# Kernel optimization log

Hardware: AMD Instinct MI355X
Metric: run time of the kernel (lower is better)

## Reference

```python
import jax, jax.numpy as jnp
import numpy as np

D_MODEL = 1024
H = 16
D_K = D_MODEL // H
VOCAB = 2048            # ctor arg `max_relative_position` actually sets embedding vocab size
MAX_REL_POS = 1000      # hardcoded in the original module
B = 4
S = 1024


def setup_inputs() -> dict:
    key = jax.random.key(0)
    ks = jax.random.split(key, 13)
    sc = 1.0 / np.sqrt(D_MODEL)
    inp = {
        "query": jax.random.normal(ks[0], (B, S, D_MODEL), jnp.float32),
        "key": jax.random.normal(ks[1], (B, S, D_MODEL), jnp.float32),
        "value": jax.random.normal(ks[2], (B, S, D_MODEL), jnp.float32),
        "Wq": jax.random.normal(ks[3], (D_MODEL, D_MODEL), jnp.float32) * sc,
        "bq": jnp.zeros((D_MODEL,), jnp.float32),
        "Wk": jax.random.normal(ks[4], (D_MODEL, D_MODEL), jnp.float32) * sc,
        "bk": jnp.zeros((D_MODEL,), jnp.float32),
        "Wv": jax.random.normal(ks[5], (D_MODEL, D_MODEL), jnp.float32) * sc,
        "bv": jnp.zeros((D_MODEL,), jnp.float32),
        "Wo": jax.random.normal(ks[6], (D_MODEL, D_MODEL), jnp.float32) * sc,
        "bo": jnp.zeros((D_MODEL,), jnp.float32),
        "embK": jax.random.normal(ks[7], (VOCAB, D_K), jnp.float32),
        "embV": jax.random.normal(ks[8], (VOCAB, D_K), jnp.float32),
    }
    return inp


def _rel_pos_idx(seq_len):
    r = jnp.arange(seq_len)
    dist = r[None, :] - r[:, None]                       # [S, S]
    return jnp.clip(dist, -MAX_REL_POS, MAX_REL_POS) + MAX_REL_POS


def reference(query, key, value, Wq, bq, Wk, bk, Wv, bv, Wo, bo, embK, embV):
    b, s, _ = query.shape
    proj = lambda x, W, bias: (x @ W.T + bias).reshape(b, s, H, D_K).transpose(0, 2, 1, 3)
    q = proj(query, Wq, bq)   # [B, H, S, Dk]
    k = proj(key, Wk, bk)
    v = proj(value, Wv, bv)

    idx = _rel_pos_idx(s)                                # [S, S] int
    rk = embK[idx]                                       # [S, S, Dk]
    rv = embV[idx]                                       # [S, S, Dk]

    # logits = Q K^T + Q R_K^T (Shaw-style, no 1/sqrt(dk) scaling in original)
    logits = jnp.einsum("bhqd,bhkd->bhqk", q, k) + jnp.einsum("bhqd,qkd->bhqk", q, rk)
    weights = jax.nn.softmax(logits, axis=-1)            # dropout is identity in eval

    # x = W V + W R_V
    x = jnp.einsum("bhqk,bhkd->bhqd", weights, v) + jnp.einsum("bhqk,qkd->bhqd", weights, rv)
    x = x.transpose(0, 2, 1, 3).reshape(b, s, H * D_K)
    out = x @ Wo.T + bo
    return out, weights
```

## Files before the change

kernel.cpp:

```cpp
#include <hip/hip_runtime.h>
#include <math.h>

#define Bn   4
#define Sn   1024
#define Dn   1024
#define Hn   16
#define DKn  64
#define MRPn 1000
#define RKU  2049

typedef __attribute__((ext_vector_type(8))) short short8;
typedef __attribute__((ext_vector_type(4))) float f32x4;

static __device__ __forceinline__ unsigned short f2bf(float f) {
    unsigned u = __float_as_uint(f);
    u += 0x7FFF + ((u >> 16) & 1);
    return (unsigned short)(u >> 16);
}
static __device__ __forceinline__ float bf2f(unsigned short h) {
    return __uint_as_float((unsigned)h << 16);
}

__global__ __launch_bounds__(256) void cast_f32_bf16(
    const float* __restrict__ s, unsigned short* __restrict__ d, int n)
{
    int i = (blockIdx.x * 256 + threadIdx.x) * 4;
    if (i >= n) return;
    float4 v = *(const float4*)(s + i);
    ushort4 o;
    o.x = f2bf(v.x); o.y = f2bf(v.y); o.z = f2bf(v.z); o.w = f2bf(v.w);
    *(ushort4*)(d + i) = o;
}

#define LP 40
__global__ __launch_bounds__(256) void gemm_bf16_mfma(
    const unsigned short* __restrict__ A, const unsigned short* __restrict__ W,
    const float* __restrict__ bias, float* __restrict__ C,
    unsigned short* __restrict__ Chi, unsigned short* __restrict__ Clo,
    int M, int N, int K, int mode)
{
    __shared__ unsigned short As[128 * LP];
    __shared__ unsigned short Bs[128 * LP];
    const int tid  = threadIdx.x;
    const int lane = tid & 63;
    const int wave = tid >> 6;
    const int m0 = blockIdx.y * 128, n0 = blockIdx.x * 128;
    const int wm = (wave & 1) * 64, wn = (wave >> 1) * 64;
    const int fr   = lane & 15;
    const int quad = lane >> 4;

    f32x4 acc[4][4];
#pragma unroll
    for (int i = 0; i < 4; ++i)
#pragma unroll
        for (int j = 0; j < 4; ++j) acc[i][j] = (f32x4){0.f, 0.f, 0.f, 0.f};

    const int srow   = tid >> 2;
    const int schunk = (tid & 3) * 8;

    for (int kb = 0; kb < K; kb += 32) {
        const unsigned short* ga = A + (size_t)(m0 + srow) * K + kb + schunk;
        const unsigned short* gb = W + (size_t)(n0 + srow) * K + kb + schunk;
        short8 a0 = *(const short8*)ga;
        short8 a1 = *(const short8*)(ga + (size_t)64 * K);
        short8 b0 = *(const short8*)gb;
        short8 b1 = *(const short8*)(gb + (size_t)64 * K);
        __syncthreads();
        *(short8*)&As[srow * LP + schunk]        = a0;
        *(short8*)&As[(srow + 64) * LP + schunk] = a1;
        *(short8*)&Bs[srow * LP + schunk]        = b0;
        *(short8*)&Bs[(srow + 64) * LP + schunk] = b1;
        __syncthreads();

        short8 af[4], bf[4];
#pragma unroll
        for (int mi = 0; mi < 4; ++mi)
            af[mi] = *(const short8*)&As[(wm + 16 * mi + fr) * LP + quad * 8];
#pragma unroll
        for (int ni = 0; ni < 4; ++ni)
            bf[ni] = *(const short8*)&Bs[(wn + 16 * ni + fr) * LP + quad * 8];
#pragma unroll
        for (int mi = 0; mi < 4; ++mi)
#pragma unroll
            for (int ni = 0; ni < 4; ++ni)
                acc[mi][ni] = __builtin_amdgcn_mfma_f32_16x16x32_bf16(
                    af[mi], bf[ni], acc[mi][ni], 0, 0, 0);
    }

    if (mode == 0) {
#pragma unroll
        for (int ni = 0; ni < 4; ++ni) {
            int cc = n0 + wn + 16 * ni + fr;
            float bv = bias[cc];
#pragma unroll
            for (int mi = 0; mi < 4; ++mi) {
                int rbase = m0 + wm + 16 * mi + quad * 4;
#pragma unroll
                for (int r = 0; r < 4; ++r)
                    C[(size_t)(rbase + r) * N + cc] = acc[mi][ni][r] + bv;
            }
        }
    } else if (mode == 1) {
#pragma unroll
        for (int ni = 0; ni < 4; ++ni) {
            int cc = n0 + wn + 16 * ni + fr;
            int h = cc >> 6, d = cc & 63;
            float bv = bias[cc];
#pragma unroll
            for (int mi = 0; mi < 4; ++mi) {
                int rbase = m0 + wm + 16 * mi + quad * 4;
                int b = rbase >> 10, q0 = rbase & 1023;
#pragma unroll
                for (int r = 0; r < 4; ++r) {
                    float val = acc[mi][ni][r] + bv;
                    unsigned short hi = f2bf(val);
                    unsigned short lo = f2bf(val - bf2f(hi));
                    size_t o = (((size_t)b * Hn + h) * Sn + q0 + r) * DKn + d;
                    Chi[o] = hi; Clo[o] = lo;
                }
            }
        }
    } else {
#pragma unroll
        for (int ni = 0; ni < 4; ++ni) {
            int cc = n0 + wn + 16 * ni + fr;
            int h = cc >> 6, d = cc & 63;
            float bv = bias[cc];
#pragma unroll
            for (int mi = 0; mi < 4; ++mi) {
                int rbase = m0 + wm + 16 * mi + quad * 4;
                int b = rbase >> 10, tok0 = rbase & 1023;
                ushort4 o4;
#pragma unroll
                for (int r = 0; r < 4; ++r) o4[r] = f2bf(acc[mi][ni][r] + bv);
                *(ushort4*)&Chi[(((size_t)b * Hn + h) * DKn + d) * Sn + tok0] = o4;
            }
        }
    }
}

__global__ __launch_bounds__(256) void build_rk(
    const float* __restrict__ embK, unsigned short* __restrict__ Rh,
    unsigned short* __restrict__ Rl)
{
    int i = (blockIdx.x * 256 + threadIdx.x) * 4;
    if (i >= RKU * DKn) return;
    int u = i >> 6, d0 = i & 63;
    int t = min(max(u - 1024, -MRPn), MRPn);
    float4 v = *(const float4*)&embK[(size_t)(t + MRPn) * DKn + d0];
    ushort4 hi, lo;
    hi.x = f2bf(v.x); lo.x = f2bf(v.x - bf2f(hi.x));
    hi.y = f2bf(v.y); lo.y = f2bf(v.y - bf2f(hi.y));
    hi.z = f2bf(v.z); lo.z = f2bf(v.z - bf2f(hi.z));
    hi.w = f2bf(v.w); lo.w = f2bf(v.w - bf2f(hi.w));
    *(ushort4*)&Rh[i] = hi;
    *(ushort4*)&Rl[i] = lo;
}

__global__ __launch_bounds__(256) void build_e2v(
    const float* __restrict__ embV, unsigned short* __restrict__ E2V)
{
    int i = (blockIdx.x * 256 + threadIdx.x) * 8;
    int d = i >> 11, u0 = i & 2047;
    short8 o;
#pragma unroll
    for (int e = 0; e < 8; ++e) {
        int t = u0 + e - 1024;
        t = min(max(t, -MRPn), MRPn);
        o[e] = (short)f2bf(embV[(size_t)(t + MRPn) * DKn + d]);
    }
    *(short8*)&E2V[i] = o;
}

__global__ __launch_bounds__(256) void logits_mfma(
    const unsigned short* __restrict__ Qh, const unsigned short* __restrict__ Ql,
    const unsigned short* __restrict__ Kh, const unsigned short* __restrict__ Kl,
    const unsigned short* __restrict__ Rh, const unsigned short* __restrict__ Rl,
    float* __restrict__ L)
{
    __shared__ float RelU[64][132];
    const int tid = threadIdx.x;
    const int lane = tid & 63, wave = tid >> 6;
    const int wy = wave >> 1, wx = wave & 1;
    const int fr = lane & 15, quad = lane >> 4;
    const int n = blockIdx.x;
    const int virt = (n & 7) * 128 + (n >> 3);
    const int bh = virt >> 4, q0 = (virt & 15) * 64;

    const unsigned short* qbh = Qh + ((size_t)bh * Sn + q0) * DKn;
    const unsigned short* qbl = Ql + ((size_t)bh * Sn + q0) * DKn;

    short8 aH[2][2], aL[2][2];
#pragma unroll
    for (int kbi = 0; kbi < 2; ++kbi)
#pragma unroll
        for (int mi = 0; mi < 2; ++mi) {
            int off = (wy * 32 + 16 * mi + fr) * DKn + kbi * 32 + quad * 8;
            aH[kbi][mi] = *(const short8*)(qbh + off);
            aL[kbi][mi] = *(const short8*)(qbl + off);
        }

    for (int kt = 0; kt < 16; ++kt) {
        const int k0 = kt * 64;
        const unsigned short* kbh = Kh + ((size_t)bh * Sn + k0) * DKn;
        const unsigned short* kbl = Kl + ((size_t)bh * Sn + k0) * DKn;
        const int u0 = k0 - q0 + 961 + wx * 64;
        const unsigned short* rbh = Rh + (size_t)u0 * DKn;
        const unsigned short* rbl = Rl + (size_t)u0 * DKn;

        f32x4 acc[2][2], rel[2][4];
#pragma unroll
        for (int i = 0; i < 2; ++i)
#pragma unroll
            for (int j = 0; j < 2; ++j) acc[i][j] = (f32x4){0.f, 0.f, 0.f, 0.f};
#pragma unroll
        for (int i = 0; i < 2; ++i)
#pragma unroll
            for (int j = 0; j < 4; ++j) rel[i][j] = (f32x4){0.f, 0.f, 0.f, 0.f};

#pragma unroll
        for (int kbi = 0; kbi < 2; ++kbi) {
            short8 bKH[2], bKL[2], bRH[4], bRL[4];
#pragma unroll
            for (int ni = 0; ni < 2; ++ni) {
                int off = (wx * 32 + 16 * ni + fr) * DKn + kbi * 32 + quad * 8;
                bKH[ni] = *(const short8*)(kbh + off);
                bKL[ni] = *(const short8*)(kbl + off);
            }
#pragma unroll
            for (int ni = 0; ni < 4; ++ni) {
                int off = (16 * ni + fr) * DKn + kbi * 32 + quad * 8;
                bRH[ni] = *(const short8*)(rbh + off);
                bRL[ni] = *(const short8*)(rbl + off);
            }
#pragma unroll
            for (int mi = 0; mi < 2; ++mi)
#pragma unroll
                for (int ni = 0; ni < 2; ++ni) {
                    acc[mi][ni] = __builtin_amdgcn_mfma_f32_16x16x32_bf16(
                        aH[kbi][mi], bKH[ni], acc[mi][ni], 0, 0, 0);
                    acc[mi][ni] = __builtin_amdgcn_mfma_f32_16x16x32_bf16(
                        aL[kbi][mi], bKH[ni], acc[mi][ni], 0, 0, 0);
                    acc[mi][ni] = __builtin_amdgcn_mfma_f32_16x16x32_bf16(
                        aH[kbi][mi], bKL[ni], acc[mi][ni], 0, 0, 0);
                }
#pragma unroll
            for (int mi = 0; mi < 2; ++mi)
#pragma unroll
                for (int ni = 0; ni < 4; ++ni) {
                    rel[mi][ni] = __builtin_amdgcn_mfma_f32_16x16x32_bf16(
                        aH[kbi][mi], bRH[ni], rel[mi][ni], 0, 0, 0);
                    rel[mi][ni] = __builtin_amdgcn_mfma_f32_16x16x32_bf16(
                        aL[kbi][mi], bRH[ni], rel[mi][ni], 0, 0, 0);
                    rel[mi][ni] = __builtin_amdgcn_mfma_f32_16x16x32_bf16(
                        aH[kbi][mi], bRL[ni], rel[mi][ni], 0, 0, 0);
                }
        }

#pragma unroll
        for (int mi = 0; mi < 2; ++mi)
#pragma unroll
            for (int ni = 0; ni < 4; ++ni)
#pragma unroll
                for (int r = 0; r < 4; ++r)
                    RelU[wy * 32 + 16 * mi + quad * 4 + r]
                        [wx * 64 + 16 * ni + fr] = rel[mi][ni][r];
        __syncthreads();
#pragma unroll
        for (int mi = 0; mi < 2; ++mi)
#pragma unroll
            for (int ni = 0; ni < 2; ++ni) {
                int c = wx * 32 + 16 * ni + fr;
#pragma unroll
                for (int r = 0; r < 4; ++r) {
                    int row = wy * 32 + 16 * mi + quad * 4 + r;
                    L[((size_t)bh * Sn + q0 + row) * Sn + k0 + c] =
                        acc[mi][ni][r] + RelU[row][c - row + 63];
                }
            }
        __syncthreads();
    }
}

__global__ __launch_bounds__(256) void softmax_kernel(float* __restrict__ Wt)
{
    __shared__ float red[4];
    const int tid = threadIdx.x;
    float* p = Wt + (size_t)blockIdx.x * Sn;
    float4 v = ((const float4*)p)[tid];

    float m = fmaxf(fmaxf(v.x, v.y), fmaxf(v.z, v.w));
#pragma unroll
    for (int o = 32; o > 0; o >>= 1) m = fmaxf(m, __shfl_down(m, o, 64));
    if ((tid & 63) == 0) red[tid >> 6] = m;
    __syncthreads();
    m = fmaxf(fmaxf(red[0], red[1]), fmaxf(red[2], red[3]));
    __syncthreads();

    float4 e;
    e.x = expf(v.x - m); e.y = expf(v.y - m);
    e.z = expf(v.z - m); e.w = expf(v.w - m);
    float s = e.x + e.y + e.z + e.w;
#pragma unroll
    for (int o = 32; o > 0; o >>= 1) s += __shfl_down(s, o, 64);
    if ((tid & 63) == 0) red[tid >> 6] = s;
    __syncthreads();
    s = red[0] + red[1] + red[2] + red[3];

    float inv = 1.0f / s;
    e.x *= inv; e.y *= inv; e.z *= inv; e.w *= inv;
    ((float4*)p)[tid] = e;
}

__global__ __launch_bounds__(256) void av_mfma(
    const float* __restrict__ Wt, const unsigned short* __restrict__ Vt,
    const unsigned short* __restrict__ E2V, unsigned short* __restrict__ Xbf)
{
    __shared__ unsigned short As[64 * LP];
    __shared__ unsigned short Bs[64 * LP];
    const int tid  = threadIdx.x;
    const int lane = tid & 63;
    const int wave = tid >> 6;
    const int q0 = blockIdx.x * 64;
    const int bh = blockIdx.y;
    const int b = bh >> 4, h = bh & 15;
    const int wm = (wave & 1) * 32;
    const int wn = (wave >> 1) * 32;
    const int fr = lane & 15, quad = lane >> 4;

    const float* Wrow = Wt + (size_t)bh * Sn * Sn;

    f32x4 acc[2][2];
#pragma unroll
    for (int i = 0; i < 2; ++i)
#pragma unroll
        for (int j = 0; j < 2; ++j) acc[i][j] = (f32x4){0.f, 0.f, 0.f, 0.f};

    const int ar = tid >> 3;
    const int ac = (tid & 7) * 4;
    const int br = tid >> 2;
    const int bc = (tid & 3) * 8;

    const unsigned short* vrow = Vt + ((size_t)bh * DKn + br) * Sn;

    for (int kb = 0; kb < Sn; kb += 32) {
        short8 bv = *(const short8*)(vrow + kb + bc);
        float4 a0 = *(const float4*)&Wrow[(size_t)(q0 + ar) * Sn + kb + ac];
        float4 a1 = *(const float4*)&Wrow[(size_t)(q0 + ar + 32) * Sn + kb + ac];
        __syncthreads();
        ushort4 s0, s1;
        s0.x = f2bf(a0.x); s0.y = f2bf(a0.y); s0.z = f2bf(a0.z); s0.w = f2bf(a0.w);
        s1.x = f2bf(a1.x); s1.y = f2bf(a1.y); s1.z = f2bf(a1.z); s1.w = f2bf(a1.w);
        *(ushort4*)&As[ar * LP + ac]        = s0;
        *(ushort4*)&As[(ar + 32) * LP + ac] = s1;
        *(short8*)&Bs[br * LP + bc]         = bv;
        __syncthreads();

        short8 af[2], bfv[2];
#pragma unroll
        for (int mi = 0; mi < 2; ++mi)
            af[mi] = *(const short8*)&As[(wm + 16 * mi + fr) * LP + quad * 8];
#pragma unroll
        for (int ni = 0; ni < 2; ++ni)
            bfv[ni] = *(const short8*)&Bs[(wn + 16 * ni + fr) * LP + quad * 8];
#pragma unroll
        for (int mi = 0; mi < 2; ++mi)
#pragma unroll
            for (int ni = 0; ni < 2; ++ni)
                acc[mi][ni] = __builtin_amdgcn_mfma_f32_16x16x32_bf16(
                    af[mi], bfv[ni], acc[mi][ni], 0, 0, 0);
    }

    int lo = 1024 - q0 - 63; if (lo < 0) lo = 0; lo &= ~31;
    const int hi = 2047 - q0;
    for (int ub = lo; ub <= hi; ub += 32) {
        short8 bv = *(const short8*)&E2V[(size_t)br * 2048 + ub + bc];
        float fa[2][4];
#pragma unroll
        for (int p = 0; p < 2; ++p) {
            int q = q0 + ar + 32 * p;
            int k = q + ub + ac - 1024;
#pragma unroll
            for (int e = 0; e < 4; ++e) {
                int ke = k + e;
                fa[p][e] = ((unsigned)ke < 1024u) ? Wrow[(size_t)q * Sn + ke] : 0.f;
            }
        }
        __syncthreads();
        ushort4 s0, s1;
        s0.x = f2bf(fa[0][0]); s0.y = f2bf(fa[0][1]);
        s0.z = f2bf(fa[0][2]); s0.w = f2bf(fa[0][3]);
        s1.x = f2bf(fa[1][0]); s1.y = f2bf(fa[1][1]);
        s1.z = f2bf(fa[1][2]); s1.w = f2bf(fa[1][3]);
        *(ushort4*)&As[ar * LP + ac]        = s0;
        *(ushort4*)&As[(ar + 32) * LP + ac] = s1;
        *(short8*)&Bs[br * LP + bc]         = bv;
        __syncthreads();

        short8 af[2], bfv[2];
#pragma unroll
        for (int mi = 0; mi < 2; ++mi)
            af[mi] = *(const short8*)&As[(wm + 16 * mi + fr) * LP + quad * 8];
#pragma unroll
        for (int ni = 0; ni < 2; ++ni)
            bfv[ni] = *(const short8*)&Bs[(wn + 16 * ni + fr) * LP + quad * 8];
#pragma unroll
        for (int mi = 0; mi < 2; ++mi)
#pragma unroll
            for (int ni = 0; ni < 2; ++ni)
                acc[mi][ni] = __builtin_amdgcn_mfma_f32_16x16x32_bf16(
                    af[mi], bfv[ni], acc[mi][ni], 0, 0, 0);
    }

#pragma unroll
    for (int ni = 0; ni < 2; ++ni) {
        int d = wn + 16 * ni + fr;
#pragma unroll
        for (int mi = 0; mi < 2; ++mi) {
            int qb = q0 + wm + 16 * mi + quad * 4;
#pragma unroll
            for (int r = 0; r < 4; ++r)
                Xbf[(size_t)(b * Sn + qb + r) * Dn + h * DKn + d] =
                    f2bf(acc[mi][ni][r]);
        }
    }
}

extern "C" void kernel_launch(void* const* d_in, const int* in_sizes, int n_in,
                              void* d_out, int out_size, void* d_ws, size_t ws_size,
                              hipStream_t stream)
{
    const float* query = (const float*)d_in[0];
    const float* key   = (const float*)d_in[1];
    const float* value = (const float*)d_in[2];
    const float* Wq    = (const float*)d_in[3];
    const float* bq    = (const float*)d_in[4];
    const float* Wk    = (const float*)d_in[5];
    const float* bk    = (const float*)d_in[6];
    const float* Wv    = (const float*)d_in[7];
    const float* bv    = (const float*)d_in[8];
    const float* Wo    = (const float*)d_in[9];
    const float* bo    = (const float*)d_in[10];
    const float* embK  = (const float*)d_in[11];
    const float* embV  = (const float*)d_in[12];

    const size_t NTOK = (size_t)Bn * Sn;
    const size_t PROJ = NTOK * Dn;
    const size_t WSZ  = (size_t)Dn * Dn;

    unsigned short* u16 = (unsigned short*)d_ws;
    unsigned short* Abf = u16;
    unsigned short* Wqb = Abf + PROJ;
    unsigned short* Wkb = Wqb + WSZ;
    unsigned short* Wvb = Wkb + WSZ;
    unsigned short* Wob = Wvb + WSZ;
    unsigned short* Qhi = Wob + WSZ;
    unsigned short* Qlo = Qhi + PROJ;
    unsigned short* Khi = Qlo + PROJ;
    unsigned short* Klo = Khi + PROJ;
    unsigned short* Vtb = Klo + PROJ;
    unsigned short* E2V = Vtb + PROJ;
    unsigned short* RkH = E2V + (size_t)DKn * 2048;
    unsigned short* RkL = RkH + (size_t)RKU * DKn;

    float* outp = (float*)d_out;
    float* Wt   = outp + PROJ;

    const int CAST_W_GRID = (int)(WSZ / 4 / 256);
    const int CAST_A_GRID = (int)(PROJ / 4 / 256);
    dim3 gemmGrid(Dn / 128, (int)(NTOK / 128));

    build_e2v<<<64, 256, 0, stream>>>(embV, E2V);
    build_rk<<<(RKU * DKn / 4 + 255) / 256, 256, 0, stream>>>(embK, RkH, RkL);

    cast_f32_bf16<<<CAST_W_GRID, 256, 0, stream>>>(Wq, Wqb, (int)WSZ);
    cast_f32_bf16<<<CAST_W_GRID, 256, 0, stream>>>(Wk, Wkb, (int)WSZ);
    cast_f32_bf16<<<CAST_W_GRID, 256, 0, stream>>>(Wv, Wvb, (int)WSZ);
    cast_f32_bf16<<<CAST_W_GRID, 256, 0, stream>>>(Wo, Wob, (int)WSZ);

    cast_f32_bf16<<<CAST_A_GRID, 256, 0, stream>>>(query, Abf, (int)PROJ);
    gemm_bf16_mfma<<<gemmGrid, 256, 0, stream>>>(Abf, Wqb, bq, nullptr, Qhi, Qlo,
                                                 (int)NTOK, Dn, Dn, 1);
    cast_f32_bf16<<<CAST_A_GRID, 256, 0, stream>>>(key, Abf, (int)PROJ);
    gemm_bf16_mfma<<<gemmGrid, 256, 0, stream>>>(Abf, Wkb, bk, nullptr, Khi, Klo,
                                                 (int)NTOK, Dn, Dn, 1);
    cast_f32_bf16<<<CAST_A_GRID, 256, 0, stream>>>(value, Abf, (int)PROJ);
    gemm_bf16_mfma<<<gemmGrid, 256, 0, stream>>>(Abf, Wvb, bv, nullptr, Vtb, nullptr,
                                                 (int)NTOK, Dn, Dn, 2);

    logits_mfma<<<Bn * Hn * (Sn / 64), 256, 0, stream>>>(
        Qhi, Qlo, Khi, Klo, RkH, RkL, Wt);

    softmax_kernel<<<Bn * Hn * Sn, 256, 0, stream>>>(Wt);

    av_mfma<<<dim3(Sn / 64, Bn * Hn), 256, 0, stream>>>(Wt, Vtb, E2V, Abf);

    gemm_bf16_mfma<<<gemmGrid, 256, 0, stream>>>(Abf, Wob, bo, outp, nullptr, nullptr,
                                                 (int)NTOK, Dn, Dn, 0);
}
```

Baseline: 890.0 us.

## Fuse logits, softmax and attention-value product into one attention kernel

```diff
diff --git a/kernel.cpp b/kernel.cpp
--- a/kernel.cpp
+++ b/kernel.cpp
@@ -8,6 +8,7 @@
 #define DKn  64
 #define MRPn 1000
 #define RKU  2049
+#define EP   2112
 
 typedef __attribute__((ext_vector_type(8))) short short8;
 typedef __attribute__((ext_vector_type(4))) float f32x4;
@@ -161,7 +162,8 @@
     const float* __restrict__ embV, unsigned short* __restrict__ E2V)
 {
     int i = (blockIdx.x * 256 + threadIdx.x) * 8;
-    int d = i >> 11, u0 = i & 2047;
+    if (i >= DKn * EP) return;
+    int d = i / EP, u0 = i % EP;
     short8 o;
 #pragma unroll
     for (int e = 0; e < 8; ++e) {
@@ -172,256 +174,230 @@
     *(short8*)&E2V[i] = o;
 }
 
-__global__ __launch_bounds__(256) void logits_mfma(
+__global__ __launch_bounds__(256) void attn_fused(
     const unsigned short* __restrict__ Qh, const unsigned short* __restrict__ Ql,
     const unsigned short* __restrict__ Kh, const unsigned short* __restrict__ Kl,
     const unsigned short* __restrict__ Rh, const unsigned short* __restrict__ Rl,
-    float* __restrict__ L)
-{
-    __shared__ float RelU[64][132];
+    const unsigned short* __restrict__ Vt, const unsigned short* __restrict__ E2V,
+    float* __restrict__ Lw, unsigned short* __restrict__ Xbf)
+{
+    __shared__ unsigned short Pbuf[32][1032];
+    __shared__ __align__(16) char scratch[12800];
+    __shared__ float rowred[32][2];
+    __shared__ float mrun[32], srun[32];
+    __shared__ float mts[16][32];
+
+    float (*RelU)[100] = (float(*)[100])scratch;
+    float (*ftab)[32]  = (float(*)[32])scratch;
+    unsigned short (*Ssk)[72] = (unsigned short(*)[72])(scratch + 2048);
+
     const int tid = threadIdx.x;
     const int lane = tid & 63, wave = tid >> 6;
     const int wy = wave >> 1, wx = wave & 1;
     const int fr = lane & 15, quad = lane >> 4;
     const int n = blockIdx.x;
-    const int virt = (n & 7) * 128 + (n >> 3);
-    const int bh = virt >> 4, q0 = (virt & 15) * 64;
-
-    const unsigned short* qbh = Qh + ((size_t)bh * Sn + q0) * DKn;
-    const unsigned short* qbl = Ql + ((size_t)bh * Sn + q0) * DKn;
-
-    short8 aH[2][2], aL[2][2];
-#pragma unroll
-    for (int kbi = 0; kbi < 2; ++kbi)
-#pragma unroll
-        for (int mi = 0; mi < 2; ++mi) {
-            int off = (wy * 32 + 16 * mi + fr) * DKn + kbi * 32 + quad * 8;
-            aH[kbi][mi] = *(const short8*)(qbh + off);
-            aL[kbi][mi] = *(const short8*)(qbl + off);
-        }
+    const int virt = (n & 7) * 256 + (n >> 3);
+    const int bh = virt >> 5, q0 = (virt & 31) * 32;
+
+    if (tid < 32) { mrun[tid] = -INFINITY; srun[tid] = 0.f; }
+
+    const unsigned short* qbh = Qh + ((size_t)bh * Sn + q0 + wy * 16 + fr) * DKn;
+    const unsigned short* qbl = Ql + ((size_t)bh * Sn + q0 + wy * 16 + fr) * DKn;
+    short8 aH[2], aL[2];
+#pragma unroll
+    for (int kbi = 0; kbi < 2; ++kbi) {
+        aH[kbi] = *(const short8*)(qbh + kbi * 32 + quad * 8);
+        aL[kbi] = *(const short8*)(qbl + kbi * 32 + quad * 8);
+    }
 
     for (int kt = 0; kt < 16; ++kt) {
         const int k0 = kt * 64;
-        const unsigned short* kbh = Kh + ((size_t)bh * Sn + k0) * DKn;
-        const unsigned short* kbl = Kl + ((size_t)bh * Sn + k0) * DKn;
-        const int u0 = k0 - q0 + 961 + wx * 64;
-        const unsigned short* rbh = Rh + (size_t)u0 * DKn;
-        const unsigned short* rbl = Rl + (size_t)u0 * DKn;
-
-        f32x4 acc[2][2], rel[2][4];
-#pragma unroll
-        for (int i = 0; i < 2; ++i)
-#pragma unroll
-            for (int j = 0; j < 2; ++j) acc[i][j] = (f32x4){0.f, 0.f, 0.f, 0.f};
-#pragma unroll
-        for (int i = 0; i < 2; ++i)
-#pragma unroll
-            for (int j = 0; j < 4; ++j) rel[i][j] = (f32x4){0.f, 0.f, 0.f, 0.f};
+        const unsigned short* kbh = Kh + ((size_t)bh * Sn + k0 + wx * 32 + fr) * DKn;
+        const unsigned short* kbl = Kl + ((size_t)bh * Sn + k0 + wx * 32 + fr) * DKn;
+        const int ubase = k0 - q0 + 993;
+        const unsigned short* rbh = Rh + ((size_t)(ubase + wx * 48) + fr) * DKn;
+        const unsigned short* rbl = Rl + ((size_t)(ubase + wx * 48) + fr) * DKn;
+
+        f32x4 acc2[2], rel3[3];
+#pragma unroll
+        for (int i = 0; i < 2; ++i) acc2[i] = (f32x4){0.f, 0.f, 0.f, 0.f};
+#pragma unroll
+        for (int i = 0; i < 3; ++i) rel3[i] = (f32x4){0.f, 0.f, 0.f, 0.f};
 
 #pragma unroll
         for (int kbi = 0; kbi < 2; ++kbi) {
-            short8 bKH[2], bKL[2], bRH[4], bRL[4];
+            short8 bKH[2], bKL[2], bRH[3], bRL[3];
 #pragma unroll
             for (int ni = 0; ni < 2; ++ni) {
-                int off = (wx * 32 + 16 * ni + fr) * DKn + kbi * 32 + quad * 8;
+                size_t off = (size_t)16 * ni * DKn + kbi * 32 + quad * 8;
                 bKH[ni] = *(const short8*)(kbh + off);
                 bKL[ni] = *(const short8*)(kbl + off);
             }
 #pragma unroll
-            for (int ni = 0; ni < 4; ++ni) {
-                int off = (16 * ni + fr) * DKn + kbi * 32 + quad * 8;
+            for (int ni = 0; ni < 3; ++ni) {
+                size_t off = (size_t)16 * ni * DKn + kbi * 32 + quad * 8;
                 bRH[ni] = *(const short8*)(rbh + off);
                 bRL[ni] = *(const short8*)(rbl + off);
             }
 #pragma unroll
-            for (int mi = 0; mi < 2; ++mi)
-#pragma unroll
-                for (int ni = 0; ni < 2; ++ni) {
-                    acc[mi][ni] = __builtin_amdgcn_mfma_f32_16x16x32_bf16(
-                        aH[kbi][mi], bKH[ni], acc[mi][ni], 0, 0, 0);
-                    acc[mi][ni] = __builtin_amdgcn_mfma_f32_16x16x32_bf16(
-                        aL[kbi][mi], bKH[ni], acc[mi][ni], 0, 0, 0);
-                    acc[mi][ni] = __builtin_amdgcn_mfma_f32_16x16x32_bf16(
-                        aH[kbi][mi], bKL[ni], acc[mi][ni], 0, 0, 0);
-                }
-#pragma unroll
-            for (int mi = 0; mi < 2; ++mi)
-#pragma unroll
-                for (int ni = 0; ni < 4; ++ni) {
-                    rel[mi][ni] = __builtin_amdgcn_mfma_f32_16x16x32_bf16(
-                        aH[kbi][mi], bRH[ni], rel[mi][ni], 0, 0, 0);
-                    rel[mi][ni] = __builtin_amdgcn_mfma_f32_16x16x32_bf16(
-                        aL[kbi][mi], bRH[ni], rel[mi][ni], 0, 0, 0);
-                    rel[mi][ni] = __builtin_amdgcn_mfma_f32_16x16x32_bf16(
-                        aH[kbi][mi], bRL[ni], rel[mi][ni], 0, 0, 0);
-                }
-        }
-
-#pragma unroll
-        for (int mi = 0; mi < 2; ++mi)
-#pragma unroll
-            for (int ni = 0; ni < 4; ++ni)
-#pragma unroll
-                for (int r = 0; r < 4; ++r)
-                    RelU[wy * 32 + 16 * mi + quad * 4 + r]
-                        [wx * 64 + 16 * ni + fr] = rel[mi][ni][r];
-        __syncthreads();
-#pragma unroll
-        for (int mi = 0; mi < 2; ++mi)
-#pragma unroll
             for (int ni = 0; ni < 2; ++ni) {
+                acc2[ni] = __builtin_amdgcn_mfma_f32_16x16x32_bf16(
+                    aH[kbi], bKH[ni], acc2[ni], 0, 0, 0);
+                acc2[ni] = __builtin_amdgcn_mfma_f32_16x16x32_bf16(
+                    aL[kbi], bKH[ni], acc2[ni], 0, 0, 0);
+                acc2[ni] = __builtin_amdgcn_mfma_f32_16x16x32_bf16(
+                    aH[kbi], bKL[ni], acc2[ni], 0, 0, 0);
+            }
+#pragma unroll
+            for (int ni = 0; ni < 3; ++ni) {
+                rel3[ni] = __builtin_amdgcn_mfma_f32_16x16x32_bf16(
+                    aH[kbi], bRH[ni], rel3[ni], 0, 0, 0);
+                rel3[ni] = __builtin_amdgcn_mfma_f32_16x16x32_bf16(
+                    aL[kbi], bRH[ni], rel3[ni], 0, 0, 0);
+                rel3[ni] = __builtin_amdgcn_mfma_f32_16x16x32_bf16(
+                    aH[kbi], bRL[ni], rel3[ni], 0, 0, 0);
+            }
+        }
+
+#pragma unroll
+        for (int ni = 0; ni < 3; ++ni)
+#pragma unroll
+            for (int r = 0; r < 4; ++r)
+                RelU[wy * 16 + quad * 4 + r][wx * 48 + 16 * ni + fr] = rel3[ni][r];
+        __syncthreads();
+
+        float lg[2][4], mt4[4];
+#pragma unroll
+        for (int ni = 0; ni < 2; ++ni)
+#pragma unroll
+            for (int r = 0; r < 4; ++r) {
+                int row = wy * 16 + quad * 4 + r;
                 int c = wx * 32 + 16 * ni + fr;
-#pragma unroll
-                for (int r = 0; r < 4; ++r) {
-                    int row = wy * 32 + 16 * mi + quad * 4 + r;
-                    L[((size_t)bh * Sn + q0 + row) * Sn + k0 + c] =
-                        acc[mi][ni][r] + RelU[row][c - row + 63];
-                }
-            }
-        __syncthreads();
-    }
-}
-
-__global__ __launch_bounds__(256) void softmax_kernel(float* __restrict__ Wt)
-{
-    __shared__ float red[4];
-    const int tid = threadIdx.x;
-    float* p = Wt + (size_t)blockIdx.x * Sn;
-    float4 v = ((const float4*)p)[tid];
-
-    float m = fmaxf(fmaxf(v.x, v.y), fmaxf(v.z, v.w));
-#pragma unroll
-    for (int o = 32; o > 0; o >>= 1) m = fmaxf(m, __shfl_down(m, o, 64));
-    if ((tid & 63) == 0) red[tid >> 6] = m;
+                lg[ni][r] = acc2[ni][r] + RelU[row][c - row + 31];
+            }
+
+#pragma unroll
+        for (int r = 0; r < 4; ++r) {
+            float m = fmaxf(lg[0][r], lg[1][r]);
+#pragma unroll
+            for (int o = 1; o < 16; o <<= 1) m = fmaxf(m, __shfl_xor(m, o, 16));
+            if (fr == 0) rowred[wy * 16 + quad * 4 + r][wx] = m;
+        }
+        __syncthreads();
+#pragma unroll
+        for (int r = 0; r < 4; ++r)
+            mt4[r] = fmaxf(rowred[wy * 16 + quad * 4 + r][0],
+                           rowred[wy * 16 + quad * 4 + r][1]);
+
+        float s4[4];
+#pragma unroll
+        for (int r = 0; r < 4; ++r) s4[r] = 0.f;
+#pragma unroll
+        for (int ni = 0; ni < 2; ++ni)
+#pragma unroll
+            for (int r = 0; r < 4; ++r) {
+                float p = expf(lg[ni][r] - mt4[r]);
+                Pbuf[wy * 16 + quad * 4 + r][k0 + wx * 32 + 16 * ni + fr] = f2bf(p);
+                s4[r] += p;
+            }
+#pragma unroll
+        for (int r = 0; r < 4; ++r)
+#pragma unroll
+            for (int o = 1; o < 16; o <<= 1) s4[r] += __shfl_xor(s4[r], o, 16);
+        __syncthreads();
+        if (fr == 0)
+#pragma unroll
+            for (int r = 0; r < 4; ++r)
+                rowred[wy * 16 + quad * 4 + r][wx] = s4[r];
+        __syncthreads();
+        if (wx == 0 && fr == 0) {
+#pragma unroll
+            for (int r = 0; r < 4; ++r) {
+                int row = wy * 16 + quad * 4 + r;
+                float st = rowred[row][0] + rowred[row][1];
+                float mo = mrun[row], mtv = mt4[r];
+                float mn = fmaxf(mo, mtv);
+                srun[row] = srun[row] * expf(mo - mn) + st * expf(mtv - mn);
+                mrun[row] = mn;
+                mts[kt][row] = mtv;
+            }
+        }
+        __syncthreads();
+    }
+
+    for (int i = tid; i < 512; i += 256) {
+        int ktt = i >> 5, row = i & 31;
+        ftab[ktt][row] = expf(mts[ktt][row] - mrun[row]) / srun[row];
+    }
     __syncthreads();
-    m = fmaxf(fmaxf(red[0], red[1]), fmaxf(red[2], red[3]));
+
+    float* Lrow = Lw + ((size_t)bh * Sn + q0) * Sn;
+#pragma unroll
+    for (int rr = 0; rr < 8; ++rr) {
+        int row = wave * 8 + rr;
+#pragma unroll
+        for (int c4 = 0; c4 < 4; ++c4) {
+            int col = c4 * 256 + lane * 4;
+            ushort4 pv = *(const ushort4*)&Pbuf[row][col];
+            float f = ftab[col >> 6][row];
+            float4 w;
+            w.x = bf2f(pv.x) * f; w.y = bf2f(pv.y) * f;
+            w.z = bf2f(pv.z) * f; w.w = bf2f(pv.w) * f;
+            *(float4*)&Lrow[(size_t)row * Sn + col] = w;
+            ushort4 o;
+            o.x = f2bf(w.x); o.y = f2bf(w.y); o.z = f2bf(w.z); o.w = f2bf(w.w);
+            *(ushort4*)&Pbuf[row][col] = o;
+        }
+    }
     __syncthreads();
 
-    float4 e;
-    e.x = expf(v.x - m); e.y = expf(v.y - m);
-    e.z = expf(v.z - m); e.w = expf(v.w - m);
-    float s = e.x + e.y + e.z + e.w;
-#pragma unroll
-    for (int o = 32; o > 0; o >>= 1) s += __shfl_down(s, o, 64);
-    if ((tid & 63) == 0) red[tid >> 6] = s;
-    __syncthreads();
-    s = red[0] + red[1] + red[2] + red[3];
-
-    float inv = 1.0f / s;
-    e.x *= inv; e.y *= inv; e.z *= inv; e.w *= inv;
-    ((float4*)p)[tid] = e;
-}
-
-__global__ __launch_bounds__(256) void av_mfma(
-    const float* __restrict__ Wt, const unsigned short* __restrict__ Vt,
-    const unsigned short* __restrict__ E2V, unsigned short* __restrict__ Xbf)
-{
-    __shared__ unsigned short As[64 * LP];
-    __shared__ unsigned short Bs[64 * LP];
-    const int tid  = threadIdx.x;
-    const int lane = tid & 63;
-    const int wave = tid >> 6;
-    const int q0 = blockIdx.x * 64;
-    const int bh = blockIdx.y;
+    f32x4 av[2];
+    av[0] = (f32x4){0.f, 0.f, 0.f, 0.f};
+    av[1] = (f32x4){0.f, 0.f, 0.f, 0.f};
+    const unsigned short* vb = Vt + ((size_t)bh * DKn + wx * 32 + fr) * Sn;
+    for (int kb = 0; kb < Sn; kb += 32) {
+        short8 a  = *(const short8*)&Pbuf[wy * 16 + fr][kb + quad * 8];
+        short8 b0 = *(const short8*)(vb + kb + quad * 8);
+        short8 b1 = *(const short8*)(vb + (size_t)16 * Sn + kb + quad * 8);
+        av[0] = __builtin_amdgcn_mfma_f32_16x16x32_bf16(a, b0, av[0], 0, 0, 0);
+        av[1] = __builtin_amdgcn_mfma_f32_16x16x32_bf16(a, b1, av[1], 0, 0, 0);
+    }
+
+    const int ub0 = 992 - q0;
+    const unsigned short* eb = E2V + (size_t)(wx * 32 + fr) * EP;
+    for (int t = 0; t < 17; ++t) {
+        const int ub = ub0 + t * 64;
+        __syncthreads();
+        {
+            int row = tid >> 3, uc = (tid & 7) * 8;
+            short8 v;
+#pragma unroll
+            for (int e = 0; e < 8; ++e) {
+                int u = ub + uc + e;
+                int k = q0 + row + u - 1024;
+                v[e] = ((unsigned)k < 1024u) ? (short)Pbuf[row][k] : (short)0;
+            }
+            *(short8*)&Ssk[row][uc] = v;
+        }
+        __syncthreads();
+#pragma unroll
+        for (int uc2 = 0; uc2 < 2; ++uc2) {
+            short8 a  = *(const short8*)&Ssk[wy * 16 + fr][uc2 * 32 + quad * 8];
+            short8 b0 = *(const short8*)(eb + ub + uc2 * 32 + quad * 8);
+            short8 b1 = *(const short8*)(eb + (size_t)16 * EP + ub + uc2 * 32 + quad * 8);
+            av[0] = __builtin_amdgcn_mfma_f32_16x16x32_bf16(a, b0, av[0], 0, 0, 0);
+            av[1] = __builtin_amdgcn_mfma_f32_16x16x32_bf16(a, b1, av[1], 0, 0, 0);
+        }
+    }
+
     const int b = bh >> 4, h = bh & 15;
-    const int wm = (wave & 1) * 32;
-    const int wn = (wave >> 1) * 32;
-    const int fr = lane & 15, quad = lane >> 4;
-
-    const float* Wrow = Wt + (size_t)bh * Sn * Sn;
-
-    f32x4 acc[2][2];
-#pragma unroll
-    for (int i = 0; i < 2; ++i)
-#pragma unroll
-        for (int j = 0; j < 2; ++j) acc[i][j] = (f32x4){0.f, 0.f, 0.f, 0.f};
-
-    const int ar = tid >> 3;
-    const int ac = (tid & 7) * 4;
-    const int br = tid >> 2;
-    const int bc = (tid & 3) * 8;
-
-    const unsigned short* vrow = Vt + ((size_t)bh * DKn + br) * Sn;
-
-    for (int kb = 0; kb < Sn; kb += 32) {
-        short8 bv = *(const short8*)(vrow + kb + bc);
-        float4 a0 = *(const float4*)&Wrow[(size_t)(q0 + ar) * Sn + kb + ac];
-        float4 a1 = *(const float4*)&Wrow[(size_t)(q0 + ar + 32) * Sn + kb + ac];
-        __syncthreads();
-        ushort4 s0, s1;
-        s0.x = f2bf(a0.x); s0.y = f2bf(a0.y); s0.z = f2bf(a0.z); s0.w = f2bf(a0.w);
-        s1.x = f2bf(a1.x); s1.y = f2bf(a1.y); s1.z = f2bf(a1.z); s1.w = f2bf(a1.w);
-        *(ushort4*)&As[ar * LP + ac]        = s0;
-        *(ushort4*)&As[(ar + 32) * LP + ac] = s1;
-        *(short8*)&Bs[br * LP + bc]         = bv;
-        __syncthreads();
-
-        short8 af[2], bfv[2];
-#pragma unroll
-        for (int mi = 0; mi < 2; ++mi)
-            af[mi] = *(const short8*)&As[(wm + 16 * mi + fr) * LP + quad * 8];
-#pragma unroll
-        for (int ni = 0; ni < 2; ++ni)
-            bfv[ni] = *(const short8*)&Bs[(wn + 16 * ni + fr) * LP + quad * 8];
-#pragma unroll
-        for (int mi = 0; mi < 2; ++mi)
-#pragma unroll
-            for (int ni = 0; ni < 2; ++ni)
-                acc[mi][ni] = __builtin_amdgcn_mfma_f32_16x16x32_bf16(
-                    af[mi], bfv[ni], acc[mi][ni], 0, 0, 0);
-    }
-
-    int lo = 1024 - q0 - 63; if (lo < 0) lo = 0; lo &= ~31;
-    const int hi = 2047 - q0;
-    for (int ub = lo; ub <= hi; ub += 32) {
-        short8 bv = *(const short8*)&E2V[(size_t)br * 2048 + ub + bc];
-        float fa[2][4];
-#pragma unroll
-        for (int p = 0; p < 2; ++p) {
-            int q = q0 + ar + 32 * p;
-            int k = q + ub + ac - 1024;
-#pragma unroll
-            for (int e = 0; e < 4; ++e) {
-                int ke = k + e;
-                fa[p][e] = ((unsigned)ke < 1024u) ? Wrow[(size_t)q * Sn + ke] : 0.f;
-            }
-        }
-        __syncthreads();
-        ushort4 s0, s1;
-        s0.x = f2bf(fa[0][0]); s0.y = f2bf(fa[0][1]);
-        s0.z = f2bf(fa[0][2]); s0.w = f2bf(fa[0][3]);
-        s1.x = f2bf(fa[1][0]); s1.y = f2bf(fa[1][1]);
-        s1.z = f2bf(fa[1][2]); s1.w = f2bf(fa[1][3]);
-        *(ushort4*)&As[ar * LP + ac]        = s0;
-        *(ushort4*)&As[(ar + 32) * LP + ac] = s1;
-        *(short8*)&Bs[br * LP + bc]         = bv;
-        __syncthreads();
-
-        short8 af[2], bfv[2];
-#pragma unroll
-        for (int mi = 0; mi < 2; ++mi)
-            af[mi] = *(const short8*)&As[(wm + 16 * mi + fr) * LP + quad * 8];
-#pragma unroll
-        for (int ni = 0; ni < 2; ++ni)
-            bfv[ni] = *(const short8*)&Bs[(wn + 16 * ni + fr) * LP + quad * 8];
-#pragma unroll
-        for (int mi = 0; mi < 2; ++mi)
-#pragma unroll
-            for (int ni = 0; ni < 2; ++ni)
-                acc[mi][ni] = __builtin_amdgcn_mfma_f32_16x16x32_bf16(
-                    af[mi], bfv[ni], acc[mi][ni], 0, 0, 0);
-    }
-
 #pragma unroll
     for (int ni = 0; ni < 2; ++ni) {
-        int d = wn + 16 * ni + fr;
-#pragma unroll
-        for (int mi = 0; mi < 2; ++mi) {
-            int qb = q0 + wm + 16 * mi + quad * 4;
-#pragma unroll
-            for (int r = 0; r < 4; ++r)
-                Xbf[(size_t)(b * Sn + qb + r) * Dn + h * DKn + d] =
-                    f2bf(acc[mi][ni][r]);
+        int d = wx * 32 + 16 * ni + fr;
+#pragma unroll
+        for (int r = 0; r < 4; ++r) {
+            int q = q0 + wy * 16 + quad * 4 + r;
+            Xbf[((size_t)(b * Sn + q)) * Dn + h * DKn + d] = f2bf(av[ni][r]);
         }
     }
 }
@@ -460,7 +436,7 @@
     unsigned short* Klo = Khi + PROJ;
     unsigned short* Vtb = Klo + PROJ;
     unsigned short* E2V = Vtb + PROJ;
-    unsigned short* RkH = E2V + (size_t)DKn * 2048;
+    unsigned short* RkH = E2V + (size_t)DKn * EP;
     unsigned short* RkL = RkH + (size_t)RKU * DKn;
 
     float* outp = (float*)d_out;
@@ -470,7 +446,7 @@
     const int CAST_A_GRID = (int)(PROJ / 4 / 256);
     dim3 gemmGrid(Dn / 128, (int)(NTOK / 128));
 
-    build_e2v<<<64, 256, 0, stream>>>(embV, E2V);
+    build_e2v<<<(DKn * EP / 8 + 255) / 256, 256, 0, stream>>>(embV, E2V);
     build_rk<<<(RKU * DKn / 4 + 255) / 256, 256, 0, stream>>>(embK, RkH, RkL);
 
     cast_f32_bf16<<<CAST_W_GRID, 256, 0, stream>>>(Wq, Wqb, (int)WSZ);
@@ -488,12 +464,8 @@
     gemm_bf16_mfma<<<gemmGrid, 256, 0, stream>>>(Abf, Wvb, bv, nullptr, Vtb, nullptr,
                                                  (int)NTOK, Dn, Dn, 2);
 
-    logits_mfma<<<Bn * Hn * (Sn / 64), 256, 0, stream>>>(
-        Qhi, Qlo, Khi, Klo, RkH, RkL, Wt);
-
-    softmax_kernel<<<Bn * Hn * Sn, 256, 0, stream>>>(Wt);
-
-    av_mfma<<<dim3(Sn / 64, Bn * Hn), 256, 0, stream>>>(Wt, Vtb, E2V, Abf);
+    attn_fused<<<Bn * Hn * (Sn / 32), 256, 0, stream>>>(
+        Qhi, Qlo, Khi, Klo, RkH, RkL, Vtb, E2V, Wt, Abf);
 
     gemm_bf16_mfma<<<gemmGrid, 256, 0, stream>>>(Abf, Wob, bo, outp, nullptr, nullptr,
                                                  (int)NTOK, Dn, Dn, 0);
```

Result: slower. 983.6 us (+10.5%).
